# Kernel tuning notes

Measured on AMD Instinct MI355X. Metric: run time of the kernel, lower is better.

The kernel has to match this reference:

```python
import jax, jax.numpy as jnp
import numpy as np

B, L, D_MODEL = 2, 1024, 1024
D_STATE, D_CONV, EXPAND, HEADDIM = 64, 4, 2, 64
D_INNER = EXPAND * D_MODEL              # 2048
NHEADS = D_INNER // HEADDIM             # 32
NGROUPS = 1
CONV_DIM = D_INNER + 2 * NGROUPS * D_STATE            # 2176
D_IN_PROJ = 2 * D_INNER + 2 * NGROUPS * D_STATE + NHEADS  # 4256
RMS_EPS = 1e-6      # block nn.RMSNorm eps
GATED_EPS = 1e-5    # Mamba2 RMSNormGated eps

def _rmsnorm(x, w, eps):
    return x * jax.lax.rsqrt(jnp.mean(x * x, axis=-1, keepdims=True) + eps) * w

def _silu(x):
    return x * jax.nn.sigmoid(x)

def _mamba2(x, W_in, conv_w, conv_b, dt_bias, A_log, D_param, ssm_norm_w, W_out):
    b, l, _ = x.shape
    zxbcdt = x @ W_in.T                                   # (b,l,D_IN_PROJ)
    z = zxbcdt[..., :D_INNER]
    xBC = zxbcdt[..., D_INNER:D_INNER + CONV_DIM]
    dt = zxbcdt[..., D_INNER + CONV_DIM:]                 # (b,l,H)
    # depthwise causal conv1d (kernel D_CONV) + silu
    pad = jnp.pad(xBC, ((0, 0), (D_CONV - 1, 0), (0, 0)))
    conv = conv_b + sum(pad[:, i:i + l, :] * conv_w[:, i] for i in range(D_CONV))
    xBC = _silu(conv)
    xs = xBC[..., :D_INNER].reshape(b, l, NHEADS, HEADDIM)
    Bm = xBC[..., D_INNER:D_INNER + D_STATE]              # (b,l,N), ngroups=1
    Cm = xBC[..., D_INNER + D_STATE:]                     # (b,l,N)
    dt = jax.nn.softplus(dt + dt_bias)                    # (b,l,H)
    dA = jnp.exp(dt * (-jnp.exp(A_log)))                  # (b,l,H)
    dtx = dt[..., None] * xs                              # (b,l,H,P)

    def step(h, inp):
        dA_t, dtx_t, B_t, C_t = inp
        h = h * dA_t[:, :, None, None] + dtx_t[..., None] * B_t[:, None, None, :]
        y_t = jnp.einsum('bhpn,bn->bhp', h, C_t)
        return h, y_t

    h0 = jnp.zeros((b, NHEADS, HEADDIM, D_STATE), x.dtype)
    _, ys = jax.lax.scan(step, h0, (dA.transpose(1, 0, 2), dtx.transpose(1, 0, 2, 3),
                                    Bm.transpose(1, 0, 2), Cm.transpose(1, 0, 2)))
    y = ys.transpose(1, 0, 2, 3) + xs * D_param[None, None, :, None]
    y = y.reshape(b, l, D_INNER)
    y = _rmsnorm(y * _silu(z), ssm_norm_w, GATED_EPS)     # RMSNormGated, norm_before_gate=False
    return y @ W_out.T

def _block(x, x_d, norm_w, W_in, conv_w, conv_b, dt_bias, A_log, D_param, ssm_norm_w, W_out, w1, w2):
    # dual_residual=True, residual_scale=1.0, dropout is identity (eval)
    x_ln = _rmsnorm(x, norm_w, RMS_EPS)
    x_f = _mamba2(x_ln, W_in, conv_w, conv_b, dt_bias, A_log, D_param, ssm_norm_w, W_out)
    x_a = x + x_f
    x_f_scaled = x_f
    x_ln = _rmsnorm(x_a, norm_w, RMS_EPS)
    g = x_ln @ w1.T
    x_f = (g * jax.nn.sigmoid(g)) * (x_ln @ w2.T)         # SwiGLU
    x_a = x_a + x_f
    x_f_scaled = x_f_scaled + x_f
    return x_a, x_d + x_f_scaled

def setup_inputs() -> dict:
    key = jax.random.key(0)
    ks = jax.random.split(key, 12)
    dt = jax.random.uniform(ks[6], (NHEADS,), minval=1e-3, maxval=0.1)
    return {
        'x': jax.random.normal(ks[0], (B, L, D_MODEL), jnp.float32),
        'x_d': jax.random.normal(ks[1], (B, L, D_MODEL), jnp.float32),
        'norm_w': jnp.ones((D_MODEL,), jnp.float32),
        'W_in': jax.random.normal(ks[2], (D_IN_PROJ, D_MODEL), jnp.float32) * (D_MODEL ** -0.5),
        'conv_w': jax.random.normal(ks[3], (CONV_DIM, D_CONV), jnp.float32) * 0.2,
        'conv_b': jnp.zeros((CONV_DIM,), jnp.float32),
        'dt_bias': dt + jnp.log(-jnp.expm1(-dt)),   # inverse softplus of dt
        'A_log': jnp.log(jax.random.uniform(ks[7], (NHEADS,), minval=1.0, maxval=16.0)),
        'D_param': jnp.ones((NHEADS,), jnp.float32),
        'ssm_norm_w': jnp.ones((D_INNER,), jnp.float32),
        'W_out': jax.random.normal(ks[4], (D_MODEL, D_INNER), jnp.float32) * (D_INNER ** -0.5),
        'w1': jax.random.normal(ks[8], (D_MODEL, D_MODEL), jnp.float32) * (D_MODEL ** -0.5),
        'w2': jax.random.normal(ks[9], (D_MODEL, D_MODEL), jnp.float32) * (D_MODEL ** -0.5),
    }

def reference(x, x_d, norm_w, W_in, conv_w, conv_b, dt_bias, A_log, D_param, ssm_norm_w, W_out, w1, w2):
    return _block(x, x_d, norm_w, W_in, conv_w, conv_b, dt_bias, A_log, D_param, ssm_norm_w, W_out, w1, w2)
```

## Files before the change

### kernel.cpp

```cpp
#include <hip/hip_runtime.h>

typedef unsigned short u16;
typedef __attribute__((ext_vector_type(8))) short bf16x8;
typedef __attribute__((ext_vector_type(4))) float f32x4;

#define B_      2
#define L_      1024
#define DM      1024
#define DI      2048
#define NH      32
#define HD      64
#define DSTATE  64
#define CONVD   2176
#define DPROJ   4256
#define ZXS     4352

__device__ __forceinline__ u16 f2bf(float f) {
  union { float f; unsigned u; } v; v.f = f;
  unsigned r = v.u + 0x7fffu + ((v.u >> 16) & 1u);
  return (u16)(r >> 16);
}

__device__ __forceinline__ void load_lds16(const void* g, void* l) {
  __builtin_amdgcn_global_load_lds(
      (const __attribute__((address_space(1))) void*)g,
      (__attribute__((address_space(3))) void*)l, 16, 0, 0);
}

__device__ __forceinline__ float block_reduce_sum256(float v) {
  #pragma unroll
  for (int off = 32; off > 0; off >>= 1) v += __shfl_down(v, off, 64);
  __shared__ float red[4];
  int lane = threadIdx.x & 63, w = threadIdx.x >> 6;
  if (lane == 0) red[w] = v;
  __syncthreads();
  return red[0] + red[1] + red[2] + red[3];
}

__global__ __launch_bounds__(256) void f32_to_bf16(const float* __restrict__ in,
                                                   u16* __restrict__ out, int n4) {
  int i = blockIdx.x * 256 + threadIdx.x;
  if (i < n4) {
    float4 v = ((const float4*)in)[i];
    ((ushort4*)out)[i] = make_ushort4(f2bf(v.x), f2bf(v.y), f2bf(v.z), f2bf(v.w));
  }
}

__global__ __launch_bounds__(256) void add_rms_kernel(
    const float* __restrict__ in1, const float* __restrict__ in2,
    float* __restrict__ sum_out, const float* __restrict__ wt,
    u16* __restrict__ out, float eps) {
  const int row = blockIdx.x;
  const int c = threadIdx.x << 2;
  float4 v = *(const float4*)(in1 + (long)row * DM + c);
  if (in2) {
    float4 u = *(const float4*)(in2 + (long)row * DM + c);
    v.x += u.x; v.y += u.y; v.z += u.z; v.w += u.w;
  }
  if (sum_out) *(float4*)(sum_out + (long)row * DM + c) = v;
  float ss = v.x * v.x + v.y * v.y + v.z * v.z + v.w * v.w;
  float tot = block_reduce_sum256(ss);
  float sc = rsqrtf(tot * (1.0f / DM) + eps);
  float4 wv = *(const float4*)(wt + c);
  *(ushort4*)(out + (long)row * DM + c) =
      make_ushort4(f2bf(v.x * sc * wv.x), f2bf(v.y * sc * wv.y),
                   f2bf(v.z * sc * wv.z), f2bf(v.w * sc * wv.w));
}

template<int NJ>
__global__ __launch_bounds__(256) void gemm_lds(
    const u16* __restrict__ A, const u16* __restrict__ Bw,
    float* __restrict__ C, int N, int Nw, int K) {
  constexpr int BN = NJ * 32;
  __shared__ u16 As[128][64];
  __shared__ u16 Bs[BN][64];
  const int tid = threadIdx.x;
  const int lane = tid & 63;
  const int wave = tid >> 6;
  const int ml = lane & 15;
  const int quad = lane >> 4;
  const int wm = (wave & 1) << 6;
  const int wn = (wave >> 1) * (BN / 2);
  const long bm = (long)blockIdx.y << 7;
  const long bn = (long)blockIdx.x * BN;

  const int lr = lane >> 3;
  const int lc = (lane & 7) ^ lr;

  f32x4 acc[4][NJ];
  #pragma unroll
  for (int i = 0; i < 4; ++i)
    #pragma unroll
    for (int j = 0; j < NJ; ++j)
      acc[i][j] = (f32x4){0.f, 0.f, 0.f, 0.f};

  auto stage = [&](int kk) {
    #pragma unroll
    for (int t = 0; t < 4; ++t) {
      const int u = wave * 4 + t;
      const u16* g = A + (bm + u * 8 + lr) * K + kk + lc * 8;
      load_lds16(g, &As[u * 8][0]);
    }
    #pragma unroll
    for (int t = 0; t < NJ; ++t) {
      const int u = wave * NJ + t;
      long brow = bn + u * 8 + lr;
      if (brow >= Nw) brow = Nw - 1;
      const u16* g = Bw + brow * K + kk + lc * 8;
      load_lds16(g, &Bs[u * 8][0]);
    }
  };

  stage(0);
  for (int kt = 0; kt < K; kt += 64) {
    __syncthreads();
    #pragma unroll
    for (int ks = 0; ks < 2; ++ks) {
      const int c = ks * 4 + quad;
      const int pc = (c ^ (ml & 7)) << 3;
      bf16x8 af[4], bfr[NJ];
      #pragma unroll
      for (int i = 0; i < 4; ++i)
        af[i] = *(const bf16x8*)&As[wm + (i << 4) + ml][pc];
      #pragma unroll
      for (int j = 0; j < NJ; ++j)
        bfr[j] = *(const bf16x8*)&Bs[wn + (j << 4) + ml][pc];
      #pragma unroll
      for (int i = 0; i < 4; ++i)
        #pragma unroll
        for (int j = 0; j < NJ; ++j)
          acc[i][j] = __builtin_amdgcn_mfma_f32_16x16x32_bf16(af[i], bfr[j], acc[i][j], 0, 0, 0);
    }
    if (kt + 64 < K) {
      __syncthreads();
      stage(kt + 64);
    }
  }

  const int rquad = quad << 2;
  #pragma unroll
  for (int i = 0; i < 4; ++i) {
    const long gm = bm + wm + (i << 4) + rquad;
    #pragma unroll
    for (int j = 0; j < NJ; ++j) {
      const long gn = bn + wn + (j << 4) + ml;
      #pragma unroll
      for (int r = 0; r < 4; ++r)
        C[(gm + r) * N + gn] = acc[i][j][r];
    }
  }
}

__global__ __launch_bounds__(256) void dtA_kernel(
    const float* __restrict__ zx, const float* __restrict__ dt_bias,
    const float* __restrict__ A_log, float* __restrict__ dts,
    float* __restrict__ glog) {
  int idx = blockIdx.x * 256 + threadIdx.x;
  int h = idx & (NH - 1);
  int row = idx >> 5;
  float x = zx[(long)row * ZXS + (DI + CONVD) + h] + dt_bias[h];
  float sp = (x > 20.f) ? x : log1pf(expf(x));
  dts[idx] = sp;
  glog[idx] = -expf(A_log[h]) * sp;
}

__global__ __launch_bounds__(256) void conv_silu_kernel(
    const float* __restrict__ zx, const float* __restrict__ cw,
    const float* __restrict__ cb, float* __restrict__ xc) {
  int idx = blockIdx.x * 256 + threadIdx.x;
  if (idx >= 2048 * 544) return;
  const int c4 = (idx % 544) << 2;
  const int row = idx / 544;
  const int t = row & (L_ - 1);
  float4 acc = *(const float4*)(cb + c4);
  float4 w0 = *(const float4*)(cw + (c4 + 0) * 4);
  float4 w1v = *(const float4*)(cw + (c4 + 1) * 4);
  float4 w2v = *(const float4*)(cw + (c4 + 2) * 4);
  float4 w3v = *(const float4*)(cw + (c4 + 3) * 4);
  const float wts[4][4] = {{w0.x, w0.y, w0.z, w0.w},
                           {w1v.x, w1v.y, w1v.z, w1v.w},
                           {w2v.x, w2v.y, w2v.z, w2v.w},
                           {w3v.x, w3v.y, w3v.z, w3v.w}};
  #pragma unroll
  for (int i = 0; i < 4; ++i) {
    int tau = t - 3 + i;
    if (tau >= 0) {
      float4 xv = *(const float4*)(zx + (long)(row - t + tau) * ZXS + DI + c4);
      acc.x = fmaf(xv.x, wts[0][i], acc.x);
      acc.y = fmaf(xv.y, wts[1][i], acc.y);
      acc.z = fmaf(xv.z, wts[2][i], acc.z);
      acc.w = fmaf(xv.w, wts[3][i], acc.w);
    }
  }
  acc.x = acc.x / (1.f + expf(-acc.x));
  acc.y = acc.y / (1.f + expf(-acc.y));
  acc.z = acc.z / (1.f + expf(-acc.z));
  acc.w = acc.w / (1.f + expf(-acc.w));
  *(float4*)(xc + (long)row * CONVD + c4) = acc;
}

__global__ __launch_bounds__(256) void ssd_chunk_kernel(
    const float* __restrict__ xc, const float* __restrict__ dts,
    const float* __restrict__ glog, float* __restrict__ yss,
    float* __restrict__ Sbuf, float* __restrict__ EGbuf,
    float* __restrict__ Lam) {
  const int c = blockIdx.x & 15;
  const int h = (blockIdx.x >> 4) & 31;
  const int b = blockIdx.x >> 9;
  const int bh = b * NH + h;
  const long crow = (long)b * L_ + c * 64;
  const int tid = threadIdx.x, lane = tid & 63, wave = tid >> 6;

  __shared__ u16 Cs[64][72], Bs[64][72], Xt[64][72], Btw[64][72], Ms[64][72];
  __shared__ float Gs[64], wjL[64], dtL[64];

  if (wave == 0) {
    float g = glog[(crow + lane) * NH + h];
    float dt = dts[(crow + lane) * NH + h];
    float G = g;
    #pragma unroll
    for (int off = 1; off < 64; off <<= 1) {
      float t = __shfl_up(G, off, 64);
      if (lane >= off) G += t;
    }
    float G63 = __shfl(G, 63, 64);
    Gs[lane] = G;
    wjL[lane] = expf(G63 - G) * dt;
    dtL[lane] = dt;
    EGbuf[(bh * 16 + c) * 64 + lane] = expf(G);
    if (lane == 63) Lam[bh * 16 + c] = expf(G63);
  }
  __syncthreads();
  for (int idx = tid; idx < 1024; idx += 256) {
    int r = idx >> 4, c4 = (idx & 15) << 2;
    const float* row = xc + (crow + r) * CONVD;
    float4 xv = *(const float4*)(row + h * HD + c4);
    Xt[c4 + 0][r] = f2bf(xv.x); Xt[c4 + 1][r] = f2bf(xv.y);
    Xt[c4 + 2][r] = f2bf(xv.z); Xt[c4 + 3][r] = f2bf(xv.w);
    float4 bv = *(const float4*)(row + DI + c4);
    *(ushort4*)&Bs[r][c4] = make_ushort4(f2bf(bv.x), f2bf(bv.y), f2bf(bv.z), f2bf(bv.w));
    float w = wjL[r];
    Btw[c4 + 0][r] = f2bf(bv.x * w); Btw[c4 + 1][r] = f2bf(bv.y * w);
    Btw[c4 + 2][r] = f2bf(bv.z * w); Btw[c4 + 3][r] = f2bf(bv.w * w);
    float4 cv = *(const float4*)(row + DI + DSTATE + c4);
    *(ushort4*)&Cs[r][c4] = make_ushort4(f2bf(cv.x), f2bf(cv.y), f2bf(cv.z), f2bf(cv.w));
  }
  __syncthreads();

  const int mrow = wave * 16 + (lane & 15);
  const int quad = lane >> 4;
  f32x4 accE[4];
  #pragma unroll
  for (int j = 0; j < 4; ++j) accE[j] = (f32x4){0.f, 0.f, 0.f, 0.f};
  #pragma unroll
  for (int ks = 0; ks < 2; ++ks) {
    int k0 = ks * 32 + quad * 8;
    bf16x8 a = *(const bf16x8*)&Cs[mrow][k0];
    #pragma unroll
    for (int j = 0; j < 4; ++j) {
      bf16x8 bfr = *(const bf16x8*)&Bs[j * 16 + (lane & 15)][k0];
      accE[j] = __builtin_amdgcn_mfma_f32_16x16x32_bf16(a, bfr, accE[j], 0, 0, 0);
    }
  }
  #pragma unroll
  for (int j = 0; j < 4; ++j) {
    int jc = j * 16 + (lane & 15);
    float Gj = Gs[jc], dtj = dtL[jc];
    #pragma unroll
    for (int r = 0; r < 4; ++r) {
      int ir = wave * 16 + quad * 4 + r;
      float v = (ir >= jc) ? accE[j][r] * expf(Gs[ir] - Gj) * dtj : 0.f;
      Ms[ir][jc] = f2bf(v);
    }
  }
  __syncthreads();
  f32x4 accY[4], accS[4];
  #pragma unroll
  for (int j = 0; j < 4; ++j) { accY[j] = (f32x4){0.f,0.f,0.f,0.f}; accS[j] = (f32x4){0.f,0.f,0.f,0.f}; }
  #pragma unroll
  for (int ks = 0; ks < 2; ++ks) {
    int k0 = ks * 32 + quad * 8;
    bf16x8 aM = *(const bf16x8*)&Ms[mrow][k0];
    bf16x8 aX = *(const bf16x8*)&Xt[mrow][k0];
    #pragma unroll
    for (int j = 0; j < 4; ++j) {
      bf16x8 bX = *(const bf16x8*)&Xt[j * 16 + (lane & 15)][k0];
      bf16x8 bB = *(const bf16x8*)&Btw[j * 16 + (lane & 15)][k0];
      accY[j] = __builtin_amdgcn_mfma_f32_16x16x32_bf16(aM, bX, accY[j], 0, 0, 0);
      accS[j] = __builtin_amdgcn_mfma_f32_16x16x32_bf16(aX, bB, accS[j], 0, 0, 0);
    }
  }
  float* Sc = Sbuf + (long)(bh * 16 + c) * 4096;
  #pragma unroll
  for (int j = 0; j < 4; ++j) {
    int col = j * 16 + (lane & 15);
    #pragma unroll
    for (int r = 0; r < 4; ++r) {
      int mr = wave * 16 + quad * 4 + r;
      yss[(crow + mr) * DI + h * HD + col] = accY[j][r];
      Sc[mr * 64 + col] = accS[j][r];
    }
  }
}

__global__ __launch_bounds__(256) void ssd_combine_kernel(
    float* __restrict__ Sbuf, const float* __restrict__ Lam) {
  const int bh = blockIdx.x;
  float* base = Sbuf + (long)bh * 16 * 4096 + threadIdx.x * 16;
  float H[16];
  #pragma unroll
  for (int k = 0; k < 16; ++k) H[k] = 0.f;
  for (int cc = 0; cc < 16; ++cc) {
    float lam = Lam[bh * 16 + cc];
    float* p = base + cc * 4096;
    float tmp[16];
    #pragma unroll
    for (int k = 0; k < 16; k += 4) {
      float4 v = *(const float4*)(p + k);
      tmp[k] = v.x; tmp[k + 1] = v.y; tmp[k + 2] = v.z; tmp[k + 3] = v.w;
    }
    #pragma unroll
    for (int k = 0; k < 16; k += 4)
      *(float4*)(p + k) = make_float4(H[k], H[k + 1], H[k + 2], H[k + 3]);
    #pragma unroll
    for (int k = 0; k < 16; ++k) H[k] = fmaf(lam, H[k], tmp[k]);
  }
}

__global__ __launch_bounds__(256) void ssd_final_kernel(
    const float* __restrict__ xc, const float* __restrict__ Sbuf,
    const float* __restrict__ EGbuf, const float* __restrict__ Dp,
    float* __restrict__ yss) {
  const int c = blockIdx.x & 15;
  const int h = (blockIdx.x >> 4) & 31;
  const int b = blockIdx.x >> 9;
  const int bh = b * NH + h;
  const long crow = (long)b * L_ + c * 64;
  const int tid = threadIdx.x, lane = tid & 63, wave = tid >> 6;
  __shared__ u16 Csc[64][72], Hs[64][72];
  __shared__ float egL[64];
  if (tid < 64) egL[tid] = EGbuf[(bh * 16 + c) * 64 + tid];
  __syncthreads();
  const float* Sc = Sbuf + (long)(bh * 16 + c) * 4096;
  for (int idx = tid; idx < 1024; idx += 256) {
    int r = idx >> 4, c4 = (idx & 15) << 2;
    float4 hv = *(const float4*)(Sc + r * 64 + c4);
    *(ushort4*)&Hs[r][c4] = make_ushort4(f2bf(hv.x), f2bf(hv.y), f2bf(hv.z), f2bf(hv.w));
    float eg = egL[r];
    float4 cv = *(const float4*)(xc + (crow + r) * CONVD + DI + DSTATE + c4);
    *(ushort4*)&Csc[r][c4] = make_ushort4(f2bf(cv.x * eg), f2bf(cv.y * eg),
                                          f2bf(cv.z * eg), f2bf(cv.w * eg));
  }
  __syncthreads();
  const int mrow = wave * 16 + (lane & 15);
  const int quad = lane >> 4;
  f32x4 acc[4];
  #pragma unroll
  for (int j = 0; j < 4; ++j) acc[j] = (f32x4){0.f, 0.f, 0.f, 0.f};
  #pragma unroll
  for (int ks = 0; ks < 2; ++ks) {
    int k0 = ks * 32 + quad * 8;
    bf16x8 a = *(const bf16x8*)&Csc[mrow][k0];
    #pragma unroll
    for (int j = 0; j < 4; ++j) {
      bf16x8 bfr = *(const bf16x8*)&Hs[j * 16 + (lane & 15)][k0];
      acc[j] = __builtin_amdgcn_mfma_f32_16x16x32_bf16(a, bfr, acc[j], 0, 0, 0);
    }
  }
  const float Dh = Dp[h];
  #pragma unroll
  for (int j = 0; j < 4; ++j) {
    int p = j * 16 + (lane & 15);
    #pragma unroll
    for (int r = 0; r < 4; ++r) {
      int ir = wave * 16 + quad * 4 + r;
      long o = (crow + ir) * DI + h * HD + p;
      float xval = xc[(crow + ir) * CONVD + h * HD + p];
      yss[o] = yss[o] + acc[j][r] + Dh * xval;
    }
  }
}

__global__ __launch_bounds__(256) void gated_rms_kernel(
    const float* __restrict__ y, const float* __restrict__ zx,
    const float* __restrict__ wt, u16* __restrict__ out) {
  const int row = blockIdx.x;
  const int c = threadIdx.x << 3;
  const float* yr = y + (long)row * DI + c;
  const float* zr = zx + (long)row * ZXS + c;
  float v[8];
  float ss = 0.f;
  #pragma unroll
  for (int i = 0; i < 8; i += 4) {
    float4 y4 = *(const float4*)(yr + i);
    float4 z4 = *(const float4*)(zr + i);
    const float zz[4] = {z4.x, z4.y, z4.z, z4.w};
    const float yy[4] = {y4.x, y4.y, y4.z, y4.w};
    #pragma unroll
    for (int j = 0; j < 4; ++j) {
      float sg = zz[j] / (1.f + expf(-zz[j]));
      float val = yy[j] * sg;
      v[i + j] = val;
      ss += val * val;
    }
  }
  float tot = block_reduce_sum256(ss);
  float sc = rsqrtf(tot * (1.0f / DI) + 1e-5f);
  const float* wr = wt + c;
  *(ushort4*)(out + (long)row * DI + c) =
      make_ushort4(f2bf(v[0] * sc * wr[0]), f2bf(v[1] * sc * wr[1]),
                   f2bf(v[2] * sc * wr[2]), f2bf(v[3] * sc * wr[3]));
  *(ushort4*)(out + (long)row * DI + c + 4) =
      make_ushort4(f2bf(v[4] * sc * wr[4]), f2bf(v[5] * sc * wr[5]),
                   f2bf(v[6] * sc * wr[6]), f2bf(v[7] * sc * wr[7]));
}

__global__ __launch_bounds__(256) void final_kernel(
    const float* __restrict__ xa, const float* __restrict__ ghb,
    const float* __restrict__ xd, const float* __restrict__ xf,
    float* __restrict__ out) {
  int i = blockIdx.x * 256 + threadIdx.x;
  int row = i >> 8, col4 = i & 255;
  float4 g4 = ((const float4*)ghb)[row * 512 + col4];
  float4 h4 = ((const float4*)ghb)[row * 512 + 256 + col4];
  float4 a4 = ((const float4*)xa)[i];
  float4 d4 = ((const float4*)xd)[i];
  float4 f4 = ((const float4*)xf)[i];
  float4 o0, o1;
  float sg;
  sg = g4.x / (1.f + expf(-g4.x)); float e0 = sg * h4.x;
  sg = g4.y / (1.f + expf(-g4.y)); float e1 = sg * h4.y;
  sg = g4.z / (1.f + expf(-g4.z)); float e2 = sg * h4.z;
  sg = g4.w / (1.f + expf(-g4.w)); float e3 = sg * h4.w;
  o0.x = a4.x + e0; o0.y = a4.y + e1; o0.z = a4.z + e2; o0.w = a4.w + e3;
  o1.x = d4.x + f4.x + e0; o1.y = d4.y + f4.y + e1;
  o1.z = d4.z + f4.z + e2; o1.w = d4.w + f4.w + e3;
  ((float4*)out)[i] = o0;
  ((float4*)(out + (long)B_ * L_ * DM))[i] = o1;
}

extern "C" void kernel_launch(void* const* d_in, const int* in_sizes, int n_in,
                              void* d_out, int out_size, void* d_ws, size_t ws_size,
                              hipStream_t stream) {
  const float* x        = (const float*)d_in[0];
  const float* x_d      = (const float*)d_in[1];
  const float* norm_w   = (const float*)d_in[2];
  const float* W_in     = (const float*)d_in[3];
  const float* conv_w   = (const float*)d_in[4];
  const float* conv_b   = (const float*)d_in[5];
  const float* dt_bias  = (const float*)d_in[6];
  const float* A_log    = (const float*)d_in[7];
  const float* D_param  = (const float*)d_in[8];
  const float* ssm_w    = (const float*)d_in[9];
  const float* W_out    = (const float*)d_in[10];
  const float* w1       = (const float*)d_in[11];
  const float* w2       = (const float*)d_in[12];
  float* out = (float*)d_out;

  char* wsc = (char*)d_ws;
  size_t off = 0;
  auto alloc = [&](size_t n) { char* p = wsc + off; off += (n + 255) & ~(size_t)255; return p; };
  float* zx   = (float*)alloc((size_t)2048 * ZXS * 4);
  float* xc   = (float*)alloc((size_t)2048 * 2176 * 4);
  float* yss  = (float*)alloc((size_t)2048 * 2048 * 4);
  float* xf   = (float*)alloc((size_t)2048 * 1024 * 4);
  float* xa   = (float*)alloc((size_t)2048 * 1024 * 4);
  float* ghb  = (float*)alloc((size_t)2048 * 2048 * 4);
  float* dts  = (float*)alloc((size_t)65536 * 4);
  float* glog = (float*)alloc((size_t)65536 * 4);
  float* EGbuf= (float*)alloc((size_t)65536 * 4);
  float* Lam  = (float*)alloc((size_t)1024 * 4);
  u16* xlnb   = (u16*)alloc((size_t)2048 * 1024 * 2);
  u16* ygnb   = (u16*)alloc((size_t)2048 * 2048 * 2);
  u16* xln2b  = (u16*)alloc((size_t)2048 * 1024 * 2);
  u16* Winb   = (u16*)alloc((size_t)4256 * 1024 * 2);
  u16* Woutb  = (u16*)alloc((size_t)1024 * 2048 * 2);
  u16* w12b   = (u16*)alloc((size_t)2048 * 1024 * 2);
  float* Sbuf = ghb;

  f32_to_bf16<<<(4256 * 1024 / 4 + 255) / 256, 256, 0, stream>>>(W_in, Winb, 4256 * 1024 / 4);
  f32_to_bf16<<<(1024 * 2048 / 4 + 255) / 256, 256, 0, stream>>>(W_out, Woutb, 1024 * 2048 / 4);
  f32_to_bf16<<<(1024 * 1024 / 4 + 255) / 256, 256, 0, stream>>>(w1, w12b, 1024 * 1024 / 4);
  f32_to_bf16<<<(1024 * 1024 / 4 + 255) / 256, 256, 0, stream>>>(w2, w12b + (size_t)1024 * 1024, 1024 * 1024 / 4);

  add_rms_kernel<<<2048, 256, 0, stream>>>(x, nullptr, nullptr, norm_w, xlnb, 1e-6f);
  gemm_lds<4><<<dim3(34, 16), 256, 0, stream>>>(xlnb, Winb, zx, ZXS, 4256, 1024);
  dtA_kernel<<<256, 256, 0, stream>>>(zx, dt_bias, A_log, dts, glog);
  conv_silu_kernel<<<(2048 * 544 + 255) / 256, 256, 0, stream>>>(zx, conv_w, conv_b, xc);
  ssd_chunk_kernel<<<1024, 256, 0, stream>>>(xc, dts, glog, yss, Sbuf, EGbuf, Lam);
  ssd_combine_kernel<<<64, 256, 0, stream>>>(Sbuf, Lam);
  ssd_final_kernel<<<1024, 256, 0, stream>>>(xc, Sbuf, EGbuf, D_param, yss);
  gated_rms_kernel<<<2048, 256, 0, stream>>>(yss, zx, ssm_w, ygnb);
  gemm_lds<2><<<dim3(16, 16), 256, 0, stream>>>(ygnb, Woutb, xf, 1024, 1024, 2048);
  add_rms_kernel<<<2048, 256, 0, stream>>>(x, xf, xa, norm_w, xln2b, 1e-6f);
  gemm_lds<4><<<dim3(16, 16), 256, 0, stream>>>(xln2b, w12b, ghb, 2048, 2048, 1024);
  final_kernel<<<2048, 256, 0, stream>>>(xa, ghb, x_d, xf, out);
}
```

Before: 305.2 us.

## Double-buffer GEMM LDS, fuse MLP epilogue, merge weight casts, fold dt into SSD

The LDS GEMM loop gets double buffering: the next K tile is prefetched into a second buffer while the current one is consumed, with manual vmcnt waits and barriers. The MLP GEMM now interleaves w1 and w2 rows so that adjacent columns pair up, and applies silu-gate plus the residual adds in its epilogue. This removes the separate final kernel and the ghb round trip. The four weight-cast launches merge into one, the dt/A computation is folded into ssd_chunk, and ssd_combine is reparallelized to one element per thread over 1024 blocks. The risks are fragile hand-written waitcnt counts, doubled LDS use lowering occupancy, and a strided scalar epilogue store pattern.

Measured after the change: 288.3 us. -5.6%, faster.

```diff
diff --git a/kernel.cpp b/kernel.cpp
--- a/kernel.cpp
+++ b/kernel.cpp
@@ -37,13 +37,31 @@
   return red[0] + red[1] + red[2] + red[3];
 }
 
-__global__ __launch_bounds__(256) void f32_to_bf16(const float* __restrict__ in,
-                                                   u16* __restrict__ out, int n4) {
-  int i = blockIdx.x * 256 + threadIdx.x;
-  if (i < n4) {
-    float4 v = ((const float4*)in)[i];
-    ((ushort4*)out)[i] = make_ushort4(f2bf(v.x), f2bf(v.y), f2bf(v.z), f2bf(v.w));
-  }
+__global__ __launch_bounds__(256) void convert_weights(
+    const float* __restrict__ W_in, const float* __restrict__ W_out,
+    const float* __restrict__ w1, const float* __restrict__ w2,
+    u16* __restrict__ Winb, u16* __restrict__ Woutb, u16* __restrict__ w12b) {
+  const long R0 = 4256L * 1024 / 4;
+  const long R1 = R0 + 2048L * 1024 / 4;
+  long i = (long)blockIdx.x * 256 + threadIdx.x;
+  float4 v;
+  ushort4* dst;
+  if (i < R0) {
+    v = ((const float4*)W_in)[i];
+    dst = ((ushort4*)Winb) + i;
+  } else if (i < R1) {
+    long j = i - R0;
+    v = ((const float4*)W_out)[j];
+    dst = ((ushort4*)Woutb) + j;
+  } else {
+    long j = i - R1;
+    long row = j >> 8;
+    long col = j & 255;
+    const float* s = (row & 1) ? w2 : w1;
+    v = ((const float4*)s)[(row >> 1) * 256 + col];
+    dst = ((ushort4*)w12b) + j;
+  }
+  *dst = make_ushort4(f2bf(v.x), f2bf(v.y), f2bf(v.z), f2bf(v.w));
 }
 
 __global__ __launch_bounds__(256) void add_rms_kernel(
@@ -72,8 +90,8 @@
     const u16* __restrict__ A, const u16* __restrict__ Bw,
     float* __restrict__ C, int N, int Nw, int K) {
   constexpr int BN = NJ * 32;
-  __shared__ u16 As[128][64];
-  __shared__ u16 Bs[BN][64];
+  __shared__ u16 As[2][128][64];
+  __shared__ u16 Bs[2][BN][64];
   const int tid = threadIdx.x;
   const int lane = tid & 63;
   const int wave = tid >> 6;
@@ -94,12 +112,12 @@
     for (int j = 0; j < NJ; ++j)
       acc[i][j] = (f32x4){0.f, 0.f, 0.f, 0.f};
 
-  auto stage = [&](int kk) {
+  auto stage = [&](int kk, int buf) {
     #pragma unroll
     for (int t = 0; t < 4; ++t) {
       const int u = wave * 4 + t;
       const u16* g = A + (bm + u * 8 + lr) * K + kk + lc * 8;
-      load_lds16(g, &As[u * 8][0]);
+      load_lds16(g, &As[buf][u * 8][0]);
     }
     #pragma unroll
     for (int t = 0; t < NJ; ++t) {
@@ -107,13 +125,22 @@
       long brow = bn + u * 8 + lr;
       if (brow >= Nw) brow = Nw - 1;
       const u16* g = Bw + brow * K + kk + lc * 8;
-      load_lds16(g, &Bs[u * 8][0]);
+      load_lds16(g, &Bs[buf][u * 8][0]);
     }
   };
 
-  stage(0);
+  stage(0, 0);
+  int buf = 0;
   for (int kt = 0; kt < K; kt += 64) {
-    __syncthreads();
+    if (kt + 64 < K) {
+      stage(kt + 64, buf ^ 1);
+      if constexpr (NJ == 4)
+        asm volatile("s_waitcnt vmcnt(8)\n\ts_barrier" ::: "memory");
+      else
+        asm volatile("s_waitcnt vmcnt(6)\n\ts_barrier" ::: "memory");
+    } else {
+      asm volatile("s_waitcnt vmcnt(0)\n\ts_barrier" ::: "memory");
+    }
     #pragma unroll
     for (int ks = 0; ks < 2; ++ks) {
       const int c = ks * 4 + quad;
@@ -121,20 +148,18 @@
       bf16x8 af[4], bfr[NJ];
       #pragma unroll
       for (int i = 0; i < 4; ++i)
-        af[i] = *(const bf16x8*)&As[wm + (i << 4) + ml][pc];
+        af[i] = *(const bf16x8*)&As[buf][wm + (i << 4) + ml][pc];
       #pragma unroll
       for (int j = 0; j < NJ; ++j)
-        bfr[j] = *(const bf16x8*)&Bs[wn + (j << 4) + ml][pc];
+        bfr[j] = *(const bf16x8*)&Bs[buf][wn + (j << 4) + ml][pc];
       #pragma unroll
       for (int i = 0; i < 4; ++i)
         #pragma unroll
         for (int j = 0; j < NJ; ++j)
           acc[i][j] = __builtin_amdgcn_mfma_f32_16x16x32_bf16(af[i], bfr[j], acc[i][j], 0, 0, 0);
     }
-    if (kt + 64 < K) {
-      __syncthreads();
-      stage(kt + 64);
-    }
+    asm volatile("s_barrier" ::: "memory");
+    buf ^= 1;
   }
 
   const int rquad = quad << 2;
@@ -151,17 +176,100 @@
   }
 }
 
-__global__ __launch_bounds__(256) void dtA_kernel(
-    const float* __restrict__ zx, const float* __restrict__ dt_bias,
-    const float* __restrict__ A_log, float* __restrict__ dts,
-    float* __restrict__ glog) {
-  int idx = blockIdx.x * 256 + threadIdx.x;
-  int h = idx & (NH - 1);
-  int row = idx >> 5;
-  float x = zx[(long)row * ZXS + (DI + CONVD) + h] + dt_bias[h];
-  float sp = (x > 20.f) ? x : log1pf(expf(x));
-  dts[idx] = sp;
-  glog[idx] = -expf(A_log[h]) * sp;
+__global__ __launch_bounds__(256) void gemm_mlp_final(
+    const u16* __restrict__ A, const u16* __restrict__ Bw,
+    const float* __restrict__ xa, const float* __restrict__ xd,
+    const float* __restrict__ xf, float* __restrict__ out, int K) {
+  constexpr int NJ = 4;
+  constexpr int BN = 128;
+  __shared__ u16 As[2][128][64];
+  __shared__ u16 Bs[2][BN][64];
+  const int tid = threadIdx.x;
+  const int lane = tid & 63;
+  const int wave = tid >> 6;
+  const int ml = lane & 15;
+  const int quad = lane >> 4;
+  const int wm = (wave & 1) << 6;
+  const int wn = (wave >> 1) * 64;
+  const long bm = (long)blockIdx.y << 7;
+  const long bn = (long)blockIdx.x * BN;
+
+  const int lr = lane >> 3;
+  const int lc = (lane & 7) ^ lr;
+
+  f32x4 acc[4][NJ];
+  #pragma unroll
+  for (int i = 0; i < 4; ++i)
+    #pragma unroll
+    for (int j = 0; j < NJ; ++j)
+      acc[i][j] = (f32x4){0.f, 0.f, 0.f, 0.f};
+
+  auto stage = [&](int kk, int buf) {
+    #pragma unroll
+    for (int t = 0; t < 4; ++t) {
+      const int u = wave * 4 + t;
+      load_lds16(A + (bm + u * 8 + lr) * K + kk + lc * 8, &As[buf][u * 8][0]);
+    }
+    #pragma unroll
+    for (int t = 0; t < NJ; ++t) {
+      const int u = wave * NJ + t;
+      load_lds16(Bw + (bn + u * 8 + lr) * K + kk + lc * 8, &Bs[buf][u * 8][0]);
+    }
+  };
+
+  stage(0, 0);
+  int buf = 0;
+  for (int kt = 0; kt < K; kt += 64) {
+    if (kt + 64 < K) {
+      stage(kt + 64, buf ^ 1);
+      asm volatile("s_waitcnt vmcnt(8)\n\ts_barrier" ::: "memory");
+    } else {
+      asm volatile("s_waitcnt vmcnt(0)\n\ts_barrier" ::: "memory");
+    }
+    #pragma unroll
+    for (int ks = 0; ks < 2; ++ks) {
+      const int c = ks * 4 + quad;
+      const int pc = (c ^ (ml & 7)) << 3;
+      bf16x8 af[4], bfr[NJ];
+      #pragma unroll
+      for (int i = 0; i < 4; ++i)
+        af[i] = *(const bf16x8*)&As[buf][wm + (i << 4) + ml][pc];
+      #pragma unroll
+      for (int j = 0; j < NJ; ++j)
+        bfr[j] = *(const bf16x8*)&Bs[buf][wn + (j << 4) + ml][pc];
+      #pragma unroll
+      for (int i = 0; i < 4; ++i)
+        #pragma unroll
+        for (int j = 0; j < NJ; ++j)
+          acc[i][j] = __builtin_amdgcn_mfma_f32_16x16x32_bf16(af[i], bfr[j], acc[i][j], 0, 0, 0);
+    }
+    asm volatile("s_barrier" ::: "memory");
+    buf ^= 1;
+  }
+
+  float* out1 = out + (long)B_ * L_ * DM;
+  const int rquad = quad << 2;
+  #pragma unroll
+  for (int i = 0; i < 4; ++i) {
+    const long gm = bm + wm + (i << 4) + rquad;
+    #pragma unroll
+    for (int j = 0; j < NJ; ++j) {
+      const long gn = bn + wn + (j << 4) + ml;
+      #pragma unroll
+      for (int r = 0; r < 4; ++r) {
+        float v = acc[i][j][r];
+        float p = __shfl_xor(v, 1, 64);
+        if ((ml & 1) == 0) {
+          float e = (v / (1.f + expf(-v))) * p;
+          long row = gm + r;
+          long col = gn >> 1;
+          long o = row * DM + col;
+          out[o]  = xa[o] + e;
+          out1[o] = xd[o] + xf[o] + e;
+        }
+      }
+    }
+  }
 }
 
 __global__ __launch_bounds__(256) void conv_silu_kernel(
@@ -200,10 +308,10 @@
 }
 
 __global__ __launch_bounds__(256) void ssd_chunk_kernel(
-    const float* __restrict__ xc, const float* __restrict__ dts,
-    const float* __restrict__ glog, float* __restrict__ yss,
-    float* __restrict__ Sbuf, float* __restrict__ EGbuf,
-    float* __restrict__ Lam) {
+    const float* __restrict__ xc, const float* __restrict__ zx,
+    const float* __restrict__ dt_bias, const float* __restrict__ A_log,
+    float* __restrict__ yss, float* __restrict__ Sbuf,
+    float* __restrict__ EGbuf, float* __restrict__ Lam) {
   const int c = blockIdx.x & 15;
   const int h = (blockIdx.x >> 4) & 31;
   const int b = blockIdx.x >> 9;
@@ -215,8 +323,9 @@
   __shared__ float Gs[64], wjL[64], dtL[64];
 
   if (wave == 0) {
-    float g = glog[(crow + lane) * NH + h];
-    float dt = dts[(crow + lane) * NH + h];
+    float draw = zx[(crow + lane) * ZXS + (DI + CONVD) + h] + dt_bias[h];
+    float dt = (draw > 20.f) ? draw : log1pf(expf(draw));
+    float g = -expf(A_log[h]) * dt;
     float G = g;
     #pragma unroll
     for (int off = 1; off < 64; off <<= 1) {
@@ -305,25 +414,16 @@
 
 __global__ __launch_bounds__(256) void ssd_combine_kernel(
     float* __restrict__ Sbuf, const float* __restrict__ Lam) {
-  const int bh = blockIdx.x;
-  float* base = Sbuf + (long)bh * 16 * 4096 + threadIdx.x * 16;
-  float H[16];
-  #pragma unroll
-  for (int k = 0; k < 16; ++k) H[k] = 0.f;
+  const int bh = blockIdx.x >> 4;
+  const int e = (blockIdx.x & 15) * 256 + threadIdx.x;
+  float* base = Sbuf + (long)bh * 16 * 4096 + e;
+  const float* lamp = Lam + bh * 16;
+  float H = 0.f;
   for (int cc = 0; cc < 16; ++cc) {
-    float lam = Lam[bh * 16 + cc];
-    float* p = base + cc * 4096;
-    float tmp[16];
-    #pragma unroll
-    for (int k = 0; k < 16; k += 4) {
-      float4 v = *(const float4*)(p + k);
-      tmp[k] = v.x; tmp[k + 1] = v.y; tmp[k + 2] = v.z; tmp[k + 3] = v.w;
-    }
-    #pragma unroll
-    for (int k = 0; k < 16; k += 4)
-      *(float4*)(p + k) = make_float4(H[k], H[k + 1], H[k + 2], H[k + 3]);
-    #pragma unroll
-    for (int k = 0; k < 16; ++k) H[k] = fmaf(lam, H[k], tmp[k]);
+    float lam = lamp[cc];
+    float v = base[cc * 4096];
+    base[cc * 4096] = H;
+    H = fmaf(lam, H, v);
   }
 }
 
@@ -415,30 +515,6 @@
                    f2bf(v[6] * sc * wr[6]), f2bf(v[7] * sc * wr[7]));
 }
 
-__global__ __launch_bounds__(256) void final_kernel(
-    const float* __restrict__ xa, const float* __restrict__ ghb,
-    const float* __restrict__ xd, const float* __restrict__ xf,
-    float* __restrict__ out) {
-  int i = blockIdx.x * 256 + threadIdx.x;
-  int row = i >> 8, col4 = i & 255;
-  float4 g4 = ((const float4*)ghb)[row * 512 + col4];
-  float4 h4 = ((const float4*)ghb)[row * 512 + 256 + col4];
-  float4 a4 = ((const float4*)xa)[i];
-  float4 d4 = ((const float4*)xd)[i];
-  float4 f4 = ((const float4*)xf)[i];
-  float4 o0, o1;
-  float sg;
-  sg = g4.x / (1.f + expf(-g4.x)); float e0 = sg * h4.x;
-  sg = g4.y / (1.f + expf(-g4.y)); float e1 = sg * h4.y;
-  sg = g4.z / (1.f + expf(-g4.z)); float e2 = sg * h4.z;
-  sg = g4.w / (1.f + expf(-g4.w)); float e3 = sg * h4.w;
-  o0.x = a4.x + e0; o0.y = a4.y + e1; o0.z = a4.z + e2; o0.w = a4.w + e3;
-  o1.x = d4.x + f4.x + e0; o1.y = d4.y + f4.y + e1;
-  o1.z = d4.z + f4.z + e2; o1.w = d4.w + f4.w + e3;
-  ((float4*)out)[i] = o0;
-  ((float4*)(out + (long)B_ * L_ * DM))[i] = o1;
-}
-
 extern "C" void kernel_launch(void* const* d_in, const int* in_sizes, int n_in,
                               void* d_out, int out_size, void* d_ws, size_t ws_size,
                               hipStream_t stream) {
@@ -465,9 +541,7 @@
   float* yss  = (float*)alloc((size_t)2048 * 2048 * 4);
   float* xf   = (float*)alloc((size_t)2048 * 1024 * 4);
   float* xa   = (float*)alloc((size_t)2048 * 1024 * 4);
-  float* ghb  = (float*)alloc((size_t)2048 * 2048 * 4);
-  float* dts  = (float*)alloc((size_t)65536 * 4);
-  float* glog = (float*)alloc((size_t)65536 * 4);
+  float* Sbuf = (float*)alloc((size_t)1024 * 16 * 4096 / 16 * 4);
   float* EGbuf= (float*)alloc((size_t)65536 * 4);
   float* Lam  = (float*)alloc((size_t)1024 * 4);
   u16* xlnb   = (u16*)alloc((size_t)2048 * 1024 * 2);
@@ -476,23 +550,16 @@
   u16* Winb   = (u16*)alloc((size_t)4256 * 1024 * 2);
   u16* Woutb  = (u16*)alloc((size_t)1024 * 2048 * 2);
   u16* w12b   = (u16*)alloc((size_t)2048 * 1024 * 2);
-  float* Sbuf = ghb;
-
-  f32_to_bf16<<<(4256 * 1024 / 4 + 255) / 256, 256, 0, stream>>>(W_in, Winb, 4256 * 1024 / 4);
-  f32_to_bf16<<<(1024 * 2048 / 4 + 255) / 256, 256, 0, stream>>>(W_out, Woutb, 1024 * 2048 / 4);
-  f32_to_bf16<<<(1024 * 1024 / 4 + 255) / 256, 256, 0, stream>>>(w1, w12b, 1024 * 1024 / 4);
-  f32_to_bf16<<<(1024 * 1024 / 4 + 255) / 256, 256, 0, stream>>>(w2, w12b + (size_t)1024 * 1024, 1024 * 1024 / 4);
-
+
+  convert_weights<<<8352, 256, 0, stream>>>(W_in, W_out, w1, w2, Winb, Woutb, w12b);
   add_rms_kernel<<<2048, 256, 0, stream>>>(x, nullptr, nullptr, norm_w, xlnb, 1e-6f);
   gemm_lds<4><<<dim3(34, 16), 256, 0, stream>>>(xlnb, Winb, zx, ZXS, 4256, 1024);
-  dtA_kernel<<<256, 256, 0, stream>>>(zx, dt_bias, A_log, dts, glog);
   conv_silu_kernel<<<(2048 * 544 + 255) / 256, 256, 0, stream>>>(zx, conv_w, conv_b, xc);
-  ssd_chunk_kernel<<<1024, 256, 0, stream>>>(xc, dts, glog, yss, Sbuf, EGbuf, Lam);
-  ssd_combine_kernel<<<64, 256, 0, stream>>>(Sbuf, Lam);
+  ssd_chunk_kernel<<<1024, 256, 0, stream>>>(xc, zx, dt_bias, A_log, yss, Sbuf, EGbuf, Lam);
+  ssd_combine_kernel<<<1024, 256, 0, stream>>>(Sbuf, Lam);
   ssd_final_kernel<<<1024, 256, 0, stream>>>(xc, Sbuf, EGbuf, D_param, yss);
   gated_rms_kernel<<<2048, 256, 0, stream>>>(yss, zx, ssm_w, ygnb);
   gemm_lds<2><<<dim3(16, 16), 256, 0, stream>>>(ygnb, Woutb, xf, 1024, 1024, 2048);
   add_rms_kernel<<<2048, 256, 0, stream>>>(x, xf, xa, norm_w, xln2b, 1e-6f);
-  gemm_lds<4><<<dim3(16, 16), 256, 0, stream>>>(xln2b, w12b, ghb, 2048, 2048, 1024);
-  final_kernel<<<2048, 256, 0, stream>>>(xa, ghb, x_d, xf, out);
-}
+  gemm_mlp_final<<<dim3(16, 16), 256, 0, stream>>>(xln2b, w12b, xa, x_d, xf, out, 1024);
+}
```
